# Optimization experiments

Measured on AMD Instinct MI355X. Metric: run time of the kernel, lower is better.

## Reference

```python
import jax, jax.numpy as jnp
import numpy as np

N_NODES = 100000
K = 5
C = 16
E = 3200000  # nonzeros per shift power


def setup_inputs() -> dict:
    key = jax.random.key(0)
    k1, k2, k3, k4, k5 = jax.random.split(key, 5)
    X = jax.random.normal(k1, (N_NODES, C), dtype=jnp.float32)
    rows = jax.random.randint(k2, (K, E), 0, N_NODES, dtype=jnp.int32)
    cols = jax.random.randint(k3, (K, E), 0, N_NODES, dtype=jnp.int32)
    vals = jax.random.normal(k4, (K, E), dtype=jnp.float32)
    h = jax.random.normal(k5, (C, K), dtype=jnp.float32)  # per-channel filter taps
    return {"X": X, "rows": rows, "cols": cols, "vals": vals, "h": h}


def reference(X, rows, cols, vals, h):
    # Original math: y = sum_c sum_k h[c,k] * (S_k @ X[:, c])
    #              = sum_k S_k @ (X @ h[:, k])
    N = X.shape[0]
    Kp, Ep = rows.shape
    Z = X @ h  # [N, K] combined per-tap signals
    # gather Z at source nodes for each tap: Zg[k, e] = Z[cols[k, e], k]
    Zg = Z[cols, jnp.arange(Kp, dtype=cols.dtype)[:, None]]  # [K, E]
    contrib = vals * Zg  # [K, E]
    y = jax.ops.segment_sum(contrib.reshape(-1), rows.reshape(-1), num_segments=N)
    return y  # [N]
```

## Files before the change

kernel.cpp:

```cpp
#include <hip/hip_runtime.h>
#include <hip/hip_fp16.h>

#define N_NODES 100000
#define KK 5
#define CC 16
#define EE 3200000
#define NXCC 8

#define NB 16
#define ROWS_PB 6250
#define WCAP 512
#define BPB 96
#define CHUNK 5120
#define NCHUNK 3125
#define GROUPS 5
#define BLK_PER_K 625

__device__ __forceinline__ int xcc_id() {
    int x;
    asm volatile("s_getreg_b32 %0, hwreg(HW_REG_XCC_ID)" : "=s"(x));
    return x & (NXCC - 1);
}

__global__ void compute_z_kernel(const float* __restrict__ X,
                                 const float* __restrict__ h,
                                 float* __restrict__ Zt) {
    int n = blockIdx.x * blockDim.x + threadIdx.x;
    if (n >= N_NODES) return;
    const float4* Xr = (const float4*)(X + (size_t)n * CC);
    float4 x0 = Xr[0], x1 = Xr[1], x2 = Xr[2], x3 = Xr[3];
    float xv[CC] = {x0.x, x0.y, x0.z, x0.w, x1.x, x1.y, x1.z, x1.w,
                    x2.x, x2.y, x2.z, x2.w, x3.x, x3.y, x3.z, x3.w};
#pragma unroll
    for (int k = 0; k < KK; ++k) {
        float acc = 0.0f;
#pragma unroll
        for (int c = 0; c < CC; ++c) acc += xv[c] * h[c * KK + k];
        Zt[k * N_NODES + n] = acc;
    }
}

__global__ void scatter_kernel(const int* __restrict__ rows,
                               const int* __restrict__ cols,
                               const float* __restrict__ vals,
                               const float* __restrict__ Zt,
                               unsigned int* __restrict__ binned,
                               int* __restrict__ counts,
                               float* __restrict__ spill) {
    __shared__ int lcnt[NB];
    int tid = threadIdx.x;
    if (tid < NB) lcnt[tid] = 0;
    __syncthreads();

    int w = blockIdx.x;
    int cbase = w * CHUNK;
    const float* Zk = Zt + (size_t)(w / BLK_PER_K) * N_NODES;
    unsigned int* wbase = binned + (size_t)w * (NB * WCAP);

#pragma unroll
    for (int g = 0; g < GROUPS; ++g) {
        int e = cbase + (g * 256 + tid) * 4;
        int4   r = *(const int4*)(rows + e);
        int4   c = *(const int4*)(cols + e);
        float4 v = *(const float4*)(vals + e);
        int   rr[4] = {r.x, r.y, r.z, r.w};
        float cb[4] = {v.x * Zk[c.x], v.y * Zk[c.y], v.z * Zk[c.z], v.w * Zk[c.w]};
#pragma unroll
        for (int i = 0; i < 4; ++i) {
            int b = rr[i] / ROWS_PB;
            int pos = atomicAdd(&lcnt[b], 1);
            if (pos < WCAP) {
                unsigned int packed =
                    ((unsigned)(rr[i] - b * ROWS_PB) << 16) |
                    (unsigned)__half_as_ushort(__float2half_rn(cb[i]));
                wbase[b * WCAP + pos] = packed;
            } else {
                unsafeAtomicAdd(&spill[rr[i]], cb[i]);
            }
        }
    }
    __syncthreads();
    if (tid < NB) counts[w * NB + tid] = min(lcnt[tid], WCAP);
}

__global__ void accum_kernel(const unsigned int* __restrict__ binned,
                             const int* __restrict__ counts,
                             float* __restrict__ partials) {
    __shared__ float acc[ROWS_PB];
    int b = blockIdx.x / BPB;
    int s = blockIdx.x % BPB;
    int tid = threadIdx.x;
    for (int i = tid; i < ROWS_PB; i += 256) acc[i] = 0.0f;
    __syncthreads();

    int wlo = (NCHUNK * s) / BPB;
    int whi = (NCHUNK * (s + 1)) / BPB;
    for (int w = wlo; w < whi; ++w) {
        int cnt = counts[w * NB + b];
        const unsigned int* src = binned + (size_t)w * (NB * WCAP) + b * WCAP;
        for (int i = tid; i < cnt; i += 256) {
            unsigned int e = src[i];
            float v = __half2float(__ushort_as_half((unsigned short)(e & 0xFFFFu)));
            atomicAdd(&acc[e >> 16], v);
        }
    }
    __syncthreads();
    float* dst = partials + (size_t)blockIdx.x * ROWS_PB;
    for (int i = tid; i < ROWS_PB; i += 256) dst[i] = acc[i];
}

__global__ void reduce_kernel(const float* __restrict__ partials,
                              const float* __restrict__ spill,
                              float* __restrict__ y) {
    int n = blockIdx.x * blockDim.x + threadIdx.x;
    if (n >= N_NODES) return;
    int b = n / ROWS_PB, loc = n - b * ROWS_PB;
    const float* p = partials + (size_t)(b * BPB) * ROWS_PB + loc;
    float acc = spill[n];
#pragma unroll 8
    for (int s = 0; s < BPB; ++s) acc += p[(size_t)s * ROWS_PB];
    y[n] = acc;
}

__global__ void edge_kernel_atomic(const int* __restrict__ rows,
                                   const int* __restrict__ cols,
                                   const float* __restrict__ vals,
                                   const float* __restrict__ Zt,
                                   float* __restrict__ yrep) {
    int t = blockIdx.x * blockDim.x + threadIdx.x;
    int base = t * 4;
    if (base >= KK * EE) return;
    int k = base / EE;
    const float* Zk = Zt + (size_t)k * N_NODES;
    float* y = yrep + (size_t)xcc_id() * N_NODES;
    int4 r = *(const int4*)(rows + base);
    int4 c = *(const int4*)(cols + base);
    float4 v = *(const float4*)(vals + base);
    unsafeAtomicAdd(&y[r.x], v.x * Zk[c.x]);
    unsafeAtomicAdd(&y[r.y], v.y * Zk[c.y]);
    unsafeAtomicAdd(&y[r.z], v.z * Zk[c.z]);
    unsafeAtomicAdd(&y[r.w], v.w * Zk[c.w]);
}

__global__ void reduce8_kernel(const float* __restrict__ yrep, float* __restrict__ y) {
    int n = blockIdx.x * blockDim.x + threadIdx.x;
    if (n >= N_NODES) return;
    float acc = 0.0f;
#pragma unroll
    for (int r = 0; r < NXCC; ++r) acc += yrep[(size_t)r * N_NODES + n];
    y[n] = acc;
}

extern "C" void kernel_launch(void* const* d_in, const int* in_sizes, int n_in,
                              void* d_out, int out_size, void* d_ws, size_t ws_size,
                              hipStream_t stream) {
    const float* X    = (const float*)d_in[0];
    const int*   rows = (const int*)  d_in[1];
    const int*   cols = (const int*)  d_in[2];
    const float* vals = (const float*)d_in[3];
    const float* h    = (const float*)d_in[4];
    float* y = (float*)d_out;

    char* ws = (char*)d_ws;
    float* Zt = (float*)ws;
    size_t counts_off  = 2000000;
    size_t spill_off   = counts_off + 200000;
    size_t binned_off  = spill_off + 400000;
    size_t binned_sz   = (size_t)NCHUNK * NB * WCAP * 4;
    size_t partial_off = binned_off + binned_sz;
    size_t partial_sz  = (size_t)NB * BPB * ROWS_PB * 4;
    size_t need = partial_off + partial_sz;

    {
        int threads = 256;
        int blocks  = (N_NODES + threads - 1) / threads;
        compute_z_kernel<<<blocks, threads, 0, stream>>>(X, h, Zt);
    }

    if (ws_size >= need) {
        int*          counts   = (int*)(ws + counts_off);
        float*        spill    = (float*)(ws + spill_off);
        unsigned int* binned   = (unsigned int*)(ws + binned_off);
        float*        partials = (float*)(ws + partial_off);
        hipMemsetAsync(spill, 0, 400000, stream);
        scatter_kernel<<<NCHUNK, 256, 0, stream>>>(rows, cols, vals, Zt,
                                                   binned, counts, spill);
        accum_kernel<<<NB * BPB, 256, 0, stream>>>(binned, counts, partials);
        {
            int threads = 256;
            int blocks  = (N_NODES + threads - 1) / threads;
            reduce_kernel<<<blocks, threads, 0, stream>>>(partials, spill, y);
        }
    } else {
        float* yrep = (float*)(ws + spill_off);
        hipMemsetAsync(yrep, 0, (size_t)NXCC * N_NODES * sizeof(float), stream);
        {
            int threads = 256;
            int blocks = ((KK * EE) / 4 + threads - 1) / threads;
            edge_kernel_atomic<<<blocks, threads, 0, stream>>>(rows, cols, vals, Zt, yrep);
        }
        {
            int threads = 256;
            int blocks  = (N_NODES + threads - 1) / threads;
            reduce8_kernel<<<blocks, threads, 0, stream>>>(yrep, y);
        }
    }
}
```

Before: 398.2 us.

## Batch scatter loads, transpose bin layout, and unroll accum reads across chunks

The scatter kernel now issues all coalesced edge loads first, then all Z gathers, then the LDS counter atomics, then the writes, so more memory requests are in flight at once. The binned buffer layout changes from chunk-major to bin-major, which makes each accum block's slices contiguous across chunks. The accum kernel preloads per-chunk counts into LDS and reads four chunks (up to 512 entries each) per iteration before doing the LDS atomics, which raises load-level parallelism. The cost is higher register pressure in both kernels. The accum unroll also assumes each chunk holds at most 512 entries (two per thread), which matches WCAP.

```diff
diff --git a/kernel.cpp b/kernel.cpp
--- a/kernel.cpp
+++ b/kernel.cpp
@@ -55,27 +55,54 @@
     int w = blockIdx.x;
     int cbase = w * CHUNK;
     const float* Zk = Zt + (size_t)(w / BLK_PER_K) * N_NODES;
-    unsigned int* wbase = binned + (size_t)w * (NB * WCAP);
-
+
+    int4   r4[GROUPS], c4[GROUPS];
+    float4 v4[GROUPS];
 #pragma unroll
     for (int g = 0; g < GROUPS; ++g) {
         int e = cbase + (g * 256 + tid) * 4;
-        int4   r = *(const int4*)(rows + e);
-        int4   c = *(const int4*)(cols + e);
-        float4 v = *(const float4*)(vals + e);
-        int   rr[4] = {r.x, r.y, r.z, r.w};
-        float cb[4] = {v.x * Zk[c.x], v.y * Zk[c.y], v.z * Zk[c.z], v.w * Zk[c.w]};
+        r4[g] = *(const int4*)(rows + e);
+        c4[g] = *(const int4*)(cols + e);
+        v4[g] = *(const float4*)(vals + e);
+    }
+
+    float z[GROUPS * 4];
+#pragma unroll
+    for (int g = 0; g < GROUPS; ++g) {
+        z[4 * g + 0] = Zk[c4[g].x];
+        z[4 * g + 1] = Zk[c4[g].y];
+        z[4 * g + 2] = Zk[c4[g].z];
+        z[4 * g + 3] = Zk[c4[g].w];
+    }
+
+    int pos[GROUPS * 4];
+#pragma unroll
+    for (int g = 0; g < GROUPS; ++g) {
+        int rr[4] = {r4[g].x, r4[g].y, r4[g].z, r4[g].w};
 #pragma unroll
         for (int i = 0; i < 4; ++i) {
             int b = rr[i] / ROWS_PB;
-            int pos = atomicAdd(&lcnt[b], 1);
-            if (pos < WCAP) {
+            pos[4 * g + i] = atomicAdd(&lcnt[b], 1);
+        }
+    }
+
+    unsigned int* wbase = binned + (size_t)w * WCAP;
+#pragma unroll
+    for (int g = 0; g < GROUPS; ++g) {
+        int   rr[4] = {r4[g].x, r4[g].y, r4[g].z, r4[g].w};
+        float vv[4] = {v4[g].x, v4[g].y, v4[g].z, v4[g].w};
+#pragma unroll
+        for (int i = 0; i < 4; ++i) {
+            int b = rr[i] / ROWS_PB;
+            float cb = vv[i] * z[4 * g + i];
+            int p = pos[4 * g + i];
+            if (p < WCAP) {
                 unsigned int packed =
                     ((unsigned)(rr[i] - b * ROWS_PB) << 16) |
-                    (unsigned)__half_as_ushort(__float2half_rn(cb[i]));
-                wbase[b * WCAP + pos] = packed;
+                    (unsigned)__half_as_ushort(__float2half_rn(cb));
+                wbase[(size_t)b * (NCHUNK * WCAP) + p] = packed;
             } else {
-                unsafeAtomicAdd(&spill[rr[i]], cb[i]);
+                unsafeAtomicAdd(&spill[rr[i]], cb);
             }
         }
     }
@@ -87,22 +114,35 @@
                              const int* __restrict__ counts,
                              float* __restrict__ partials) {
     __shared__ float acc[ROWS_PB];
+    __shared__ int cnts[40];
     int b = blockIdx.x / BPB;
     int s = blockIdx.x % BPB;
     int tid = threadIdx.x;
-    for (int i = tid; i < ROWS_PB; i += 256) acc[i] = 0.0f;
-    __syncthreads();
-
     int wlo = (NCHUNK * s) / BPB;
     int whi = (NCHUNK * (s + 1)) / BPB;
-    for (int w = wlo; w < whi; ++w) {
-        int cnt = counts[w * NB + b];
-        const unsigned int* src = binned + (size_t)w * (NB * WCAP) + b * WCAP;
-        for (int i = tid; i < cnt; i += 256) {
-            unsigned int e = src[i];
-            float v = __half2float(__ushort_as_half((unsigned short)(e & 0xFFFFu)));
-            atomicAdd(&acc[e >> 16], v);
-        }
+    for (int i = tid; i < ROWS_PB; i += 256) acc[i] = 0.0f;
+    if (tid < whi - wlo) cnts[tid] = counts[(wlo + tid) * NB + b];
+    __syncthreads();
+
+    const unsigned int* bbase = binned + (size_t)b * (NCHUNK * WCAP);
+    for (int w0 = wlo; w0 < whi; w0 += 4) {
+        unsigned int e[8];
+        int ok[8];
+#pragma unroll
+        for (int j = 0; j < 4; ++j) {
+            int w = w0 + j;
+            int cnt = (w < whi) ? cnts[w - wlo] : 0;
+            const unsigned int* src = bbase + (size_t)w * WCAP;
+            ok[2 * j]     = tid < cnt;
+            ok[2 * j + 1] = tid + 256 < cnt;
+            e[2 * j]      = ok[2 * j]     ? src[tid]       : 0u;
+            e[2 * j + 1]  = ok[2 * j + 1] ? src[tid + 256] : 0u;
+        }
+#pragma unroll
+        for (int q = 0; q < 8; ++q)
+            if (ok[q])
+                atomicAdd(&acc[e[q] >> 16],
+                          __half2float(__ushort_as_half((unsigned short)(e[q] & 0xFFFFu))));
     }
     __syncthreads();
     float* dst = partials + (size_t)blockIdx.x * ROWS_PB;
```

Measured after the change: 362.8 us. 1.1x faster.

## Stage binned entries in LDS and store bin-major layout for coalesced accumulation

Applied to the files above, without the earlier changes.

The scatter kernel now stages packed entries in a padded shared buffer and writes them out per bin into a bin-major global layout, so each bin's chunks are contiguous for the accumulation pass. Both kernels move to 512 threads, scatter issues all gathers up front before the LDS atomics, and accum batches 8 chunk loads per iteration with counts cached in shared memory. BPB drops from 96 to 64, which means fewer partial buffers to reduce but less parallelism in accum. The cnts array of 56 entries assumes at most 56 chunks per block slice (3125/64 ≈ 49), so it stays in bounds.

```diff
diff --git a/kernel.cpp b/kernel.cpp
--- a/kernel.cpp
+++ b/kernel.cpp
@@ -10,10 +10,10 @@
 #define NB 16
 #define ROWS_PB 6250
 #define WCAP 512
-#define BPB 96
+#define WPAD 513
+#define BPB 64
 #define CHUNK 5120
 #define NCHUNK 3125
-#define GROUPS 5
 #define BLK_PER_K 625
 
 __device__ __forceinline__ int xcc_id() {
@@ -40,14 +40,16 @@
     }
 }
 
-__global__ void scatter_kernel(const int* __restrict__ rows,
-                               const int* __restrict__ cols,
-                               const float* __restrict__ vals,
-                               const float* __restrict__ Zt,
-                               unsigned int* __restrict__ binned,
-                               int* __restrict__ counts,
-                               float* __restrict__ spill) {
+__global__ __launch_bounds__(512, 2)
+void scatter_kernel(const int* __restrict__ rows,
+                    const int* __restrict__ cols,
+                    const float* __restrict__ vals,
+                    const float* __restrict__ Zt,
+                    unsigned int* __restrict__ binned,
+                    int* __restrict__ counts,
+                    float* __restrict__ spill) {
     __shared__ int lcnt[NB];
+    __shared__ unsigned int buf[NB * WPAD];
     int tid = threadIdx.x;
     if (tid < NB) lcnt[tid] = 0;
     __syncthreads();
@@ -55,58 +57,96 @@
     int w = blockIdx.x;
     int cbase = w * CHUNK;
     const float* Zk = Zt + (size_t)(w / BLK_PER_K) * N_NODES;
-    unsigned int* wbase = binned + (size_t)w * (NB * WCAP);
-
-#pragma unroll
-    for (int g = 0; g < GROUPS; ++g) {
-        int e = cbase + (g * 256 + tid) * 4;
-        int4   r = *(const int4*)(rows + e);
-        int4   c = *(const int4*)(cols + e);
-        float4 v = *(const float4*)(vals + e);
-        int   rr[4] = {r.x, r.y, r.z, r.w};
-        float cb[4] = {v.x * Zk[c.x], v.y * Zk[c.y], v.z * Zk[c.z], v.w * Zk[c.w]};
-#pragma unroll
-        for (int i = 0; i < 4; ++i) {
-            int b = rr[i] / ROWS_PB;
-            int pos = atomicAdd(&lcnt[b], 1);
-            if (pos < WCAP) {
-                unsigned int packed =
-                    ((unsigned)(rr[i] - b * ROWS_PB) << 16) |
-                    (unsigned)__half_as_ushort(__float2half_rn(cb[i]));
-                wbase[b * WCAP + pos] = packed;
-            } else {
-                unsafeAtomicAdd(&spill[rr[i]], cb[i]);
-            }
-        }
-    }
-    __syncthreads();
+
+    int e0 = cbase + tid * 4;
+    int e1 = cbase + 2048 + tid * 4;
+    int e2 = cbase + 4096 + tid * 2;
+    int4   r0 = *(const int4*)(rows + e0);
+    int4   c0 = *(const int4*)(cols + e0);
+    float4 v0 = *(const float4*)(vals + e0);
+    int4   r1 = *(const int4*)(rows + e1);
+    int4   c1 = *(const int4*)(cols + e1);
+    float4 v1 = *(const float4*)(vals + e1);
+    int2   r2 = *(const int2*)(rows + e2);
+    int2   c2 = *(const int2*)(cols + e2);
+    float2 v2 = *(const float2*)(vals + e2);
+
+    float z[10];
+    z[0] = Zk[c0.x]; z[1] = Zk[c0.y]; z[2] = Zk[c0.z]; z[3] = Zk[c0.w];
+    z[4] = Zk[c1.x]; z[5] = Zk[c1.y]; z[6] = Zk[c1.z]; z[7] = Zk[c1.w];
+    z[8] = Zk[c2.x]; z[9] = Zk[c2.y];
+
+    int   rr[10] = {r0.x, r0.y, r0.z, r0.w, r1.x, r1.y, r1.z, r1.w, r2.x, r2.y};
+    float vv[10] = {v0.x, v0.y, v0.z, v0.w, v1.x, v1.y, v1.z, v1.w, v2.x, v2.y};
+
+    int pos[10];
+#pragma unroll
+    for (int i = 0; i < 10; ++i) {
+        int b = rr[i] / ROWS_PB;
+        pos[i] = atomicAdd(&lcnt[b], 1);
+    }
+
+#pragma unroll
+    for (int i = 0; i < 10; ++i) {
+        int b = rr[i] / ROWS_PB;
+        float cb = vv[i] * z[i];
+        int p = pos[i];
+        if (p < WCAP) {
+            unsigned int packed =
+                ((unsigned)(rr[i] - b * ROWS_PB) << 16) |
+                (unsigned)__half_as_ushort(__float2half_rn(cb));
+            buf[b * WPAD + p] = packed;
+        } else {
+            unsafeAtomicAdd(&spill[rr[i]], cb);
+        }
+    }
+    __syncthreads();
+
+    unsigned int* wbase = binned + (size_t)w * WCAP;
+#pragma unroll 1
+    for (int b = 0; b < NB; ++b) {
+        int cnt = min(lcnt[b], WCAP);
+        unsigned int* dst = wbase + (size_t)b * ((size_t)NCHUNK * WCAP);
+        if (tid < cnt) dst[tid] = buf[b * WPAD + tid];
+    }
     if (tid < NB) counts[w * NB + tid] = min(lcnt[tid], WCAP);
 }
 
-__global__ void accum_kernel(const unsigned int* __restrict__ binned,
-                             const int* __restrict__ counts,
-                             float* __restrict__ partials) {
+__global__ __launch_bounds__(512, 2)
+void accum_kernel(const unsigned int* __restrict__ binned,
+                  const int* __restrict__ counts,
+                  float* __restrict__ partials) {
     __shared__ float acc[ROWS_PB];
+    __shared__ int cnts[56];
     int b = blockIdx.x / BPB;
     int s = blockIdx.x % BPB;
     int tid = threadIdx.x;
-    for (int i = tid; i < ROWS_PB; i += 256) acc[i] = 0.0f;
-    __syncthreads();
-
     int wlo = (NCHUNK * s) / BPB;
     int whi = (NCHUNK * (s + 1)) / BPB;
-    for (int w = wlo; w < whi; ++w) {
-        int cnt = counts[w * NB + b];
-        const unsigned int* src = binned + (size_t)w * (NB * WCAP) + b * WCAP;
-        for (int i = tid; i < cnt; i += 256) {
-            unsigned int e = src[i];
-            float v = __half2float(__ushort_as_half((unsigned short)(e & 0xFFFFu)));
-            atomicAdd(&acc[e >> 16], v);
-        }
+    for (int i = tid; i < ROWS_PB; i += 512) acc[i] = 0.0f;
+    if (tid < whi - wlo) cnts[tid] = counts[(wlo + tid) * NB + b];
+    __syncthreads();
+
+    const unsigned int* bbase = binned + (size_t)b * ((size_t)NCHUNK * WCAP);
+    for (int w0 = wlo; w0 < whi; w0 += 8) {
+        unsigned int e[8];
+        int ok[8];
+#pragma unroll
+        for (int j = 0; j < 8; ++j) {
+            int w = w0 + j;
+            int cnt = (w < whi) ? cnts[w - wlo] : 0;
+            ok[j] = tid < cnt;
+            e[j]  = ok[j] ? bbase[(size_t)w * WCAP + tid] : 0u;
+        }
+#pragma unroll
+        for (int j = 0; j < 8; ++j)
+            if (ok[j])
+                atomicAdd(&acc[e[j] >> 16],
+                          __half2float(__ushort_as_half((unsigned short)(e[j] & 0xFFFFu))));
     }
     __syncthreads();
     float* dst = partials + (size_t)blockIdx.x * ROWS_PB;
-    for (int i = tid; i < ROWS_PB; i += 256) dst[i] = acc[i];
+    for (int i = tid; i < ROWS_PB; i += 512) dst[i] = acc[i];
 }
 
 __global__ void reduce_kernel(const float* __restrict__ partials,
@@ -183,9 +223,9 @@
         unsigned int* binned   = (unsigned int*)(ws + binned_off);
         float*        partials = (float*)(ws + partial_off);
         hipMemsetAsync(spill, 0, 400000, stream);
-        scatter_kernel<<<NCHUNK, 256, 0, stream>>>(rows, cols, vals, Zt,
+        scatter_kernel<<<NCHUNK, 512, 0, stream>>>(rows, cols, vals, Zt,
                                                    binned, counts, spill);
-        accum_kernel<<<NB * BPB, 256, 0, stream>>>(binned, counts, partials);
+        accum_kernel<<<NB * BPB, 512, 0, stream>>>(binned, counts, partials);
         {
             int threads = 256;
             int blocks  = (N_NODES + threads - 1) / threads;
```

New measurement: 362.1 us. 1.1x faster.

## Replace binned LDS scatter pipeline with per-XCC replicated global atomics

Applied to the files above, without the earlier changes.

Removes the binning scatter, the LDS accumulate and the partial-reduce kernels, which also quantized contributions to fp16. It always uses a single edge kernel that gathers Z and atomically adds into per-XCC replicas of y, followed by an 8-way reduce. Each thread now handles 10 edges, with all loads issued before any gathers, and the edge streams are read with nontemporal loads. The price is contention on global atomics in L2 in place of LDS atomics, but there is less intermediate memory traffic and fewer launches.

```diff
diff --git a/kernel.cpp b/kernel.cpp
--- a/kernel.cpp
+++ b/kernel.cpp
@@ -7,14 +7,14 @@
 #define EE 3200000
 #define NXCC 8
 
-#define NB 16
-#define ROWS_PB 6250
-#define WCAP 512
-#define BPB 96
-#define CHUNK 5120
-#define NCHUNK 3125
-#define GROUPS 5
-#define BLK_PER_K 625
+#define EPB 2560
+#define NBLK 6250
+#define BLKS_PER_K 1250
+
+typedef int   int4v   __attribute__((ext_vector_type(4)));
+typedef int   int2v   __attribute__((ext_vector_type(2)));
+typedef float float4v __attribute__((ext_vector_type(4)));
+typedef float float2v __attribute__((ext_vector_type(2)));
 
 __device__ __forceinline__ int xcc_id() {
     int x;
@@ -40,109 +40,52 @@
     }
 }
 
-__global__ void scatter_kernel(const int* __restrict__ rows,
-                               const int* __restrict__ cols,
-                               const float* __restrict__ vals,
-                               const float* __restrict__ Zt,
-                               unsigned int* __restrict__ binned,
-                               int* __restrict__ counts,
-                               float* __restrict__ spill) {
-    __shared__ int lcnt[NB];
-    int tid = threadIdx.x;
-    if (tid < NB) lcnt[tid] = 0;
-    __syncthreads();
+__global__ __launch_bounds__(256)
+void edge_kernel(const int* __restrict__ rows,
+                 const int* __restrict__ cols,
+                 const float* __restrict__ vals,
+                 const float* __restrict__ Zt,
+                 float* __restrict__ yrep) {
+    int tid  = threadIdx.x;
+    int b    = blockIdx.x;
+    int base = b * EPB;
+    int k    = b / BLKS_PER_K;
+    const float* Zk = Zt + (size_t)k * N_NODES;
+    float* yr = yrep + (size_t)xcc_id() * N_NODES;
 
-    int w = blockIdx.x;
-    int cbase = w * CHUNK;
-    const float* Zk = Zt + (size_t)(w / BLK_PER_K) * N_NODES;
-    unsigned int* wbase = binned + (size_t)w * (NB * WCAP);
+    int e0 = base + tid * 4;
+    int e1 = e0 + 1024;
+    int e2 = base + 2048 + tid * 2;
 
-#pragma unroll
-    for (int g = 0; g < GROUPS; ++g) {
-        int e = cbase + (g * 256 + tid) * 4;
-        int4   r = *(const int4*)(rows + e);
-        int4   c = *(const int4*)(cols + e);
-        float4 v = *(const float4*)(vals + e);
-        int   rr[4] = {r.x, r.y, r.z, r.w};
-        float cb[4] = {v.x * Zk[c.x], v.y * Zk[c.y], v.z * Zk[c.z], v.w * Zk[c.w]};
-#pragma unroll
-        for (int i = 0; i < 4; ++i) {
-            int b = rr[i] / ROWS_PB;
-            int pos = atomicAdd(&lcnt[b], 1);
-            if (pos < WCAP) {
-                unsigned int packed =
-                    ((unsigned)(rr[i] - b * ROWS_PB) << 16) |
-                    (unsigned)__half_as_ushort(__float2half_rn(cb[i]));
-                wbase[b * WCAP + pos] = packed;
-            } else {
-                unsafeAtomicAdd(&spill[rr[i]], cb[i]);
-            }
-        }
-    }
-    __syncthreads();
-    if (tid < NB) counts[w * NB + tid] = min(lcnt[tid], WCAP);
+    int4v   r0 = __builtin_nontemporal_load((const int4v*)(rows + e0));
+    int4v   c0 = __builtin_nontemporal_load((const int4v*)(cols + e0));
+    float4v v0 = __builtin_nontemporal_load((const float4v*)(vals + e0));
+    int4v   r1 = __builtin_nontemporal_load((const int4v*)(rows + e1));
+    int4v   c1 = __builtin_nontemporal_load((const int4v*)(cols + e1));
+    float4v v1 = __builtin_nontemporal_load((const float4v*)(vals + e1));
+    int2v   r2 = __builtin_nontemporal_load((const int2v*)(rows + e2));
+    int2v   c2 = __builtin_nontemporal_load((const int2v*)(cols + e2));
+    float2v v2 = __builtin_nontemporal_load((const float2v*)(vals + e2));
+
+    float z[10];
+    z[0] = Zk[c0[0]]; z[1] = Zk[c0[1]]; z[2] = Zk[c0[2]]; z[3] = Zk[c0[3]];
+    z[4] = Zk[c1[0]]; z[5] = Zk[c1[1]]; z[6] = Zk[c1[2]]; z[7] = Zk[c1[3]];
+    z[8] = Zk[c2[0]]; z[9] = Zk[c2[1]];
+
+    unsafeAtomicAdd(&yr[r0[0]], v0[0] * z[0]);
+    unsafeAtomicAdd(&yr[r0[1]], v0[1] * z[1]);
+    unsafeAtomicAdd(&yr[r0[2]], v0[2] * z[2]);
+    unsafeAtomicAdd(&yr[r0[3]], v0[3] * z[3]);
+    unsafeAtomicAdd(&yr[r1[0]], v1[0] * z[4]);
+    unsafeAtomicAdd(&yr[r1[1]], v1[1] * z[5]);
+    unsafeAtomicAdd(&yr[r1[2]], v1[2] * z[6]);
+    unsafeAtomicAdd(&yr[r1[3]], v1[3] * z[7]);
+    unsafeAtomicAdd(&yr[r2[0]], v2[0] * z[8]);
+    unsafeAtomicAdd(&yr[r2[1]], v2[1] * z[9]);
 }
 
-__global__ void accum_kernel(const unsigned int* __restrict__ binned,
-                             const int* __restrict__ counts,
-                             float* __restrict__ partials) {
-    __shared__ float acc[ROWS_PB];
-    int b = blockIdx.x / BPB;
-    int s = blockIdx.x % BPB;
-    int tid = threadIdx.x;
-    for (int i = tid; i < ROWS_PB; i += 256) acc[i] = 0.0f;
-    __syncthreads();
-
-    int wlo = (NCHUNK * s) / BPB;
-    int whi = (NCHUNK * (s + 1)) / BPB;
-    for (int w = wlo; w < whi; ++w) {
-        int cnt = counts[w * NB + b];
-        const unsigned int* src = binned + (size_t)w * (NB * WCAP) + b * WCAP;
-        for (int i = tid; i < cnt; i += 256) {
-            unsigned int e = src[i];
-            float v = __half2float(__ushort_as_half((unsigned short)(e & 0xFFFFu)));
-            atomicAdd(&acc[e >> 16], v);
-        }
-    }
-    __syncthreads();
-    float* dst = partials + (size_t)blockIdx.x * ROWS_PB;
-    for (int i = tid; i < ROWS_PB; i += 256) dst[i] = acc[i];
-}
-
-__global__ void reduce_kernel(const float* __restrict__ partials,
-                              const float* __restrict__ spill,
-                              float* __restrict__ y) {
-    int n = blockIdx.x * blockDim.x + threadIdx.x;
-    if (n >= N_NODES) return;
-    int b = n / ROWS_PB, loc = n - b * ROWS_PB;
-    const float* p = partials + (size_t)(b * BPB) * ROWS_PB + loc;
-    float acc = spill[n];
-#pragma unroll 8
-    for (int s = 0; s < BPB; ++s) acc += p[(size_t)s * ROWS_PB];
-    y[n] = acc;
-}
-
-__global__ void edge_kernel_atomic(const int* __restrict__ rows,
-                                   const int* __restrict__ cols,
-                                   const float* __restrict__ vals,
-                                   const float* __restrict__ Zt,
-                                   float* __restrict__ yrep) {
-    int t = blockIdx.x * blockDim.x + threadIdx.x;
-    int base = t * 4;
-    if (base >= KK * EE) return;
-    int k = base / EE;
-    const float* Zk = Zt + (size_t)k * N_NODES;
-    float* y = yrep + (size_t)xcc_id() * N_NODES;
-    int4 r = *(const int4*)(rows + base);
-    int4 c = *(const int4*)(cols + base);
-    float4 v = *(const float4*)(vals + base);
-    unsafeAtomicAdd(&y[r.x], v.x * Zk[c.x]);
-    unsafeAtomicAdd(&y[r.y], v.y * Zk[c.y]);
-    unsafeAtomicAdd(&y[r.z], v.z * Zk[c.z]);
-    unsafeAtomicAdd(&y[r.w], v.w * Zk[c.w]);
-}
-
-__global__ void reduce8_kernel(const float* __restrict__ yrep, float* __restrict__ y) {
+__global__ void reduce8_kernel(const float* __restrict__ yrep,
+                               float* __restrict__ y) {
     int n = blockIdx.x * blockDim.x + threadIdx.x;
     if (n >= N_NODES) return;
     float acc = 0.0f;
@@ -162,14 +105,8 @@
     float* y = (float*)d_out;
 
     char* ws = (char*)d_ws;
-    float* Zt = (float*)ws;
-    size_t counts_off  = 2000000;
-    size_t spill_off   = counts_off + 200000;
-    size_t binned_off  = spill_off + 400000;
-    size_t binned_sz   = (size_t)NCHUNK * NB * WCAP * 4;
-    size_t partial_off = binned_off + binned_sz;
-    size_t partial_sz  = (size_t)NB * BPB * ROWS_PB * 4;
-    size_t need = partial_off + partial_sz;
+    float* Zt   = (float*)ws;
+    float* yrep = (float*)(ws + 2000000);
 
     {
         int threads = 256;
@@ -177,32 +114,13 @@
         compute_z_kernel<<<blocks, threads, 0, stream>>>(X, h, Zt);
     }
 
-    if (ws_size >= need) {
-        int*          counts   = (int*)(ws + counts_off);
-        float*        spill    = (float*)(ws + spill_off);
-        unsigned int* binned   = (unsigned int*)(ws + binned_off);
-        float*        partials = (float*)(ws + partial_off);
-        hipMemsetAsync(spill, 0, 400000, stream);
-        scatter_kernel<<<NCHUNK, 256, 0, stream>>>(rows, cols, vals, Zt,
-                                                   binned, counts, spill);
-        accum_kernel<<<NB * BPB, 256, 0, stream>>>(binned, counts, partials);
-        {
-            int threads = 256;
-            int blocks  = (N_NODES + threads - 1) / threads;
-            reduce_kernel<<<blocks, threads, 0, stream>>>(partials, spill, y);
-        }
-    } else {
-        float* yrep = (float*)(ws + spill_off);
-        hipMemsetAsync(yrep, 0, (size_t)NXCC * N_NODES * sizeof(float), stream);
-        {
-            int threads = 256;
-            int blocks = ((KK * EE) / 4 + threads - 1) / threads;
-            edge_kernel_atomic<<<blocks, threads, 0, stream>>>(rows, cols, vals, Zt, yrep);
-        }
-        {
-            int threads = 256;
-            int blocks  = (N_NODES + threads - 1) / threads;
-            reduce8_kernel<<<blocks, threads, 0, stream>>>(yrep, y);
-        }
+    hipMemsetAsync(yrep, 0, (size_t)NXCC * N_NODES * sizeof(float), stream);
+
+    edge_kernel<<<NBLK, 256, 0, stream>>>(rows, cols, vals, Zt, yrep);
+
+    {
+        int threads = 256;
+        int blocks  = (N_NODES + threads - 1) / threads;
+        reduce8_kernel<<<blocks, threads, 0, stream>>>(yrep, y);
     }
 }
```

Result: slower. 928.5 us (+133.2%).
